# Kernel optimization log

Measured on AMD Instinct MI355X. Metric: run time of the kernel, lower is better.

The kernel has to match this reference:

```python
import jax, jax.numpy as jnp
import numpy as np

K = 3
PAD = 1
KK = K * K
GROUPS = 32  # min(32, dim) with dim=64
EPS = 1e-5


def _conv(x, w, pad):
    return jax.lax.conv_general_dilated(
        x, w, (1, 1), [(pad, pad), (pad, pad)],
        dimension_numbers=('NCHW', 'OIHW', 'NCHW'))


def _bilinear_gather(x, py, px):
    # x: (B,C,H,W); py,px: (B,KK,H,W) float sampling coords (zero pad outside)
    B, C, H, W = x.shape
    xf = x.reshape(B, C, H * W)
    y0f = jnp.floor(py)
    x0f = jnp.floor(px)
    wy1 = py - y0f  # fractional weights (differentiable path to offsets)
    wx1 = px - x0f
    y0 = y0f.astype(jnp.int32)
    x0 = x0f.astype(jnp.int32)

    def g(yi, xi):
        valid = (yi >= 0) & (yi < H) & (xi >= 0) & (xi < W)
        idx = (jnp.clip(yi, 0, H - 1) * W + jnp.clip(xi, 0, W - 1)).reshape(B, 1, -1)
        v = jnp.take_along_axis(xf, idx, axis=2).reshape(B, C, KK, H, W)
        return v * valid[:, None].astype(x.dtype)

    v00 = g(y0, x0)
    v01 = g(y0, x0 + 1)
    v10 = g(y0 + 1, x0)
    v11 = g(y0 + 1, x0 + 1)
    wy1e = wy1[:, None]
    wx1e = wx1[:, None]
    return (v00 * (1 - wy1e) * (1 - wx1e) + v01 * (1 - wy1e) * wx1e
            + v10 * wy1e * (1 - wx1e) + v11 * wy1e * wx1e)


def _forward(x, w_off1, w_off2, w_mask1, w_mask2, weight, bias, gamma, beta):
    B, C, H, W = x.shape
    # offset branch: 1x1 conv then KxK conv -> (B, 2*KK, H, W)
    off = _conv(_conv(x, w_off1, 0), w_off2, PAD).reshape(B, KK, 2, H, W)
    # mask branch -> sigmoid modulation (B, KK, H, W)
    mask = jax.nn.sigmoid(_conv(_conv(x, w_mask1, 0), w_mask2, PAD))
    # base kernel grid (torchvision deform_conv2d: pairs are (dy, dx) per tap)
    ky = jnp.repeat(jnp.arange(K) - PAD, K).astype(x.dtype)
    kx = jnp.tile(jnp.arange(K) - PAD, K).astype(x.dtype)
    py = off[:, :, 0] + jnp.arange(H, dtype=x.dtype)[None, None, :, None] + ky[None, :, None, None]
    px = off[:, :, 1] + jnp.arange(W, dtype=x.dtype)[None, None, None, :] + kx[None, :, None, None]
    samp = _bilinear_gather(x, py, px)  # (B, C, KK, H, W)
    # depthwise deformable conv: per-channel weight over KK taps, modulated by mask
    out = jnp.einsum('bkhw,ck,bckhw->bchw', mask, weight.reshape(C, KK), samp)
    out = out + bias[None, :, None, None]
    # GroupNorm(32, C)
    g = out.reshape(B, GROUPS, C // GROUPS, H, W)
    mu = g.mean(axis=(2, 3, 4), keepdims=True)
    var = g.var(axis=(2, 3, 4), keepdims=True)
    gn = ((g - mu) * jax.lax.rsqrt(var + EPS)).reshape(B, C, H, W)
    gn = gn * gamma[None, :, None, None] + beta[None, :, None, None]
    return jax.nn.gelu(gn, approximate=False)


def setup_inputs() -> dict:
    key = jax.random.key(0)
    ks = jax.random.split(key, 6)
    B, C, H, W = 4, 64, 128, 128
    x = jax.random.normal(ks[0], (B, C, H, W), dtype=jnp.float32)
    w_off1 = jax.random.normal(ks[1], (C, C, 1, 1), dtype=jnp.float32) * 0.05
    w_off2 = jax.random.normal(ks[2], (2 * KK, C, K, K), dtype=jnp.float32) * 0.02
    w_mask1 = jax.random.normal(ks[3], (C, C, 1, 1), dtype=jnp.float32) * 0.05
    w_mask2 = jax.random.normal(ks[4], (KK, C, K, K), dtype=jnp.float32) * 0.05
    bound = 1.0 / np.sqrt(KK)  # kaiming_uniform(a=1) for (C,1,K,K) -> fan_in=KK
    weight = jax.random.uniform(ks[5], (C, 1, K, K), dtype=jnp.float32,
                                minval=-bound, maxval=bound)
    bias = jnp.zeros((C,), dtype=jnp.float32)
    gamma = jnp.ones((C,), dtype=jnp.float32)
    beta = jnp.zeros((C,), dtype=jnp.float32)
    return {'x': x, 'w_off1': w_off1, 'w_off2': w_off2, 'w_mask1': w_mask1,
            'w_mask2': w_mask2, 'weight': weight, 'bias': bias,
            'gamma': gamma, 'beta': beta}


def reference(x, w_off1, w_off2, w_mask1, w_mask2, weight, bias, gamma, beta):
    return _forward(x, w_off1, w_off2, w_mask1, w_mask2, weight, bias, gamma, beta)
```

## Files before the change

### kernel.cpp

```cpp
#include <hip/hip_runtime.h>
#include <math.h>

#define B_  4
#define C_  64
#define H_  128
#define W_  128
#define HW_ (H_*W_)
#define NPIX_ (B_*HW_)
#define GROUPS_ 32

typedef __attribute__((ext_vector_type(8))) short short8;
typedef __attribute__((ext_vector_type(4))) float f32x4;

__device__ inline short f2bf_rne(float f) {
    unsigned u = __float_as_uint(f);
    unsigned r = (u + 0x7FFFu + ((u >> 16) & 1u)) >> 16;
    return (short)r;
}
__device__ inline short8 ld8(const short* p) {
    union { uint4 u; short8 s; } c;
    c.u = *(const uint4*)p;
    return c.s;
}

__global__ __launch_bounds__(256) void k01(const float* __restrict__ x,
                                           const float* __restrict__ w_off1,
                                           const float* __restrict__ w_mask1,
                                           const float* __restrict__ w_off2,
                                           const float* __restrict__ w_mask2,
                                           short* __restrict__ xtb,
                                           short* __restrict__ wc_hi) {
    if (blockIdx.x >= 1024) {
        int i = (blockIdx.x - 1024) * 256 + threadIdx.x;
        if (i < 32 * 576) {
            int cout = i / 576;
            int r    = i % 576;
            int pos  = r >> 6, ci = r & 63;
            float s = 0.f;
            if (cout < 18) {
                for (int cm = 0; cm < 64; cm++)
                    s += w_off2[(cout * 64 + cm) * 9 + pos] * w_off1[cm * 64 + ci];
            } else if (cout < 27) {
                for (int cm = 0; cm < 64; cm++)
                    s += w_mask2[((cout - 18) * 64 + cm) * 9 + pos] * w_mask1[cm * 64 + ci];
            }
            wc_hi[i] = f2bf_rne(s);
        }
        return;
    }
    int l   = threadIdx.x & 63;
    int wv  = threadIdx.x >> 6;
    int row = l >> 4, col = l & 15;
    int p0  = blockIdx.x * 64 + wv * 16;
    int b   = p0 >> 14;
    int hw  = p0 & (HW_ - 1);
    const float* xb = x + (size_t)b * C_ * HW_ + hw;
#pragma unroll
    for (int kb = 0; kb < 2; kb++) {
        int ci0 = kb * 32 + row * 8;
        float xv[8];
#pragma unroll
        for (int j = 0; j < 8; j++) xv[j] = xb[(ci0 + j) * HW_ + col];
        short8 a;
#pragma unroll
        for (int j = 0; j < 8; j++) a[j] = f2bf_rne(xv[j]);
        union { short8 s; uint4 u; } cv; cv.s = a;
        *(uint4*)(xtb + ((size_t)(p0 + col)) * 64 + ci0) = cv.u;
    }
}

__global__ __launch_bounds__(256, 2) void k2_mfma(const short* __restrict__ xtb,
                                                  const short* __restrict__ wc_hi,
                                                  float* __restrict__ offmask) {
    int l   = threadIdx.x & 63;
    int wv  = threadIdx.x >> 6;
    int row = l >> 4, col = l & 15;
    int blk = blockIdx.x;
    int h   = blk & 127;
    int pb  = blk * 128 + wv * 32;
    int w0  = (pb & 127);

    short8 wfr[18][2];
#pragma unroll
    for (int kb = 0; kb < 18; kb++) {
        int pos = kb >> 1;
        int ci0 = (kb & 1) * 32 + row * 8;
        int ko  = pos * 64 + ci0;
        wfr[kb][0] = ld8(wc_hi + (size_t)col * 576 + ko);
        wfr[kb][1] = ld8(wc_hi + (size_t)(col + 16) * 576 + ko);
    }

    const short8 zero = {0,0,0,0,0,0,0,0};
    f32x4 a00 = {0.f,0.f,0.f,0.f};
    f32x4 a01 = {0.f,0.f,0.f,0.f};
    f32x4 a10 = {0.f,0.f,0.f,0.f};
    f32x4 a11 = {0.f,0.f,0.f,0.f};

    short8 ca0, ca1;
    {
        const int dy = -1, dx = -1;
        int ci0 = row * 8;
#pragma unroll
        for (int mt = 0; mt < 2; mt++) {
            int pbase = pb + mt * 16 + col;
            int w = w0 + mt * 16 + col;
            bool valid = ((unsigned)(h + dy) < 128u) && ((unsigned)(w + dx) < 128u);
            int addr = valid ? (pbase + dy * 128 + dx) : pbase;
            short8 v = ld8(xtb + (size_t)addr * 64 + ci0);
            if (mt == 0) ca0 = valid ? v : zero; else ca1 = valid ? v : zero;
        }
    }

#pragma unroll
    for (int kb = 0; kb < 18; kb++) {
        short8 na0, na1;
        if (kb < 17) {
            const int kn = kb + 1;
            const int pos = kn >> 1;
            const int dy = pos / 3 - 1, dx = pos % 3 - 1;
            int ci0 = (kn & 1) * 32 + row * 8;
#pragma unroll
            for (int mt = 0; mt < 2; mt++) {
                int pbase = pb + mt * 16 + col;
                int w = w0 + mt * 16 + col;
                bool valid = ((unsigned)(h + dy) < 128u) && ((unsigned)(w + dx) < 128u);
                int addr = valid ? (pbase + dy * 128 + dx) : pbase;
                short8 v = ld8(xtb + (size_t)addr * 64 + ci0);
                if (mt == 0) na0 = valid ? v : zero; else na1 = valid ? v : zero;
            }
        }
        a00 = __builtin_amdgcn_mfma_f32_16x16x32_bf16(ca0, wfr[kb][0], a00, 0, 0, 0);
        a01 = __builtin_amdgcn_mfma_f32_16x16x32_bf16(ca0, wfr[kb][1], a01, 0, 0, 0);
        a10 = __builtin_amdgcn_mfma_f32_16x16x32_bf16(ca1, wfr[kb][0], a10, 0, 0, 0);
        a11 = __builtin_amdgcn_mfma_f32_16x16x32_bf16(ca1, wfr[kb][1], a11, 0, 0, 0);
        ca0 = na0; ca1 = na1;
    }

#pragma unroll
    for (int mt = 0; mt < 2; mt++) {
        f32x4 n0 = mt ? a10 : a00;
        f32x4 n1 = mt ? a11 : a01;
#pragma unroll
        for (int r = 0; r < 4; r++) {
            int p = pb + mt * 16 + row * 4 + r;
            float* om = offmask + (size_t)p * 32;
            om[col] = n0[r];
            if (col < 2)       om[16 + col] = n1[r];
            else if (col < 11) om[16 + col] = 1.f / (1.f + expf(-n1[r]));
        }
    }
}

__global__ __launch_bounds__(256) void k3_deform(const short* __restrict__ xtb,
                                                 const float* __restrict__ offmask,
                                                 const float* __restrict__ weight,
                                                 const float* __restrict__ bias,
                                                 unsigned short* __restrict__ out_pre,
                                                 float* __restrict__ partials) {
    __shared__ float wl[C_ * 9];
    __shared__ float bl[C_];
    __shared__ float lds_s[4][4][8];
    __shared__ float lds_ss[4][4][8];
    for (int i = threadIdx.x; i < C_ * 9; i += 256) wl[i] = weight[i];
    if (threadIdx.x < C_) bl[threadIdx.x] = bias[threadIdx.x];
    __syncthreads();

    int blk   = blockIdx.x;
    int xcd   = blk & 7;
    int slot  = blk >> 3;
    int b     = slot >> 5;
    int r     = (slot & 31) >> 1;
    int hrow  = slot & 1;
    int h     = xcd * 16 + r;
    int pl    = threadIdx.x >> 2;
    int chunk = threadIdx.x & 3;
    int c0    = chunk * 16;
    int w     = hrow * 64 + pl;
    int hw    = h * W_ + w;
    int P     = b * HW_ + hw;
    int slot_img = xcd * 32 + (slot & 31);

    float acc[16];
#pragma unroll
    for (int i = 0; i < 16; i++) acc[i] = 0.f;

    const float* po = offmask + (size_t)P * 32;
    const short* xb = xtb + (size_t)b * HW_ * 64;

    for (int k = 0; k < 9; k++) {
        float offy = po[2 * k];
        float offx = po[2 * k + 1];
        float mk   = po[18 + k];
        float py = offy + (float)h + (float)(k / 3 - 1);
        float px = offx + (float)w + (float)(k % 3 - 1);
        float y0f = floorf(py), x0f = floorf(px);
        int y0 = (int)y0f, x0 = (int)x0f;
        int y1 = y0 + 1,   x1 = x0 + 1;
        float wy1 = py - y0f, wx1 = px - x0f;
        float wy0 = 1.f - wy1, wx0 = 1.f - wx1;
        bool vy0 = ((unsigned)y0 < (unsigned)H_);
        bool vy1 = ((unsigned)y1 < (unsigned)H_);
        bool vx0 = ((unsigned)x0 < (unsigned)W_);
        bool vx1 = ((unsigned)x1 < (unsigned)W_);
        int cy0 = min(max(y0, 0), H_ - 1);
        int cy1 = min(max(y1, 0), H_ - 1);
        int cx0 = min(max(x0, 0), W_ - 1);
        int cx1 = min(max(x1, 0), W_ - 1);
        float b00 = wy0 * wx0 * ((vy0 && vx0) ? mk : 0.f);
        float b01 = wy0 * wx1 * ((vy0 && vx1) ? mk : 0.f);
        float b10 = wy1 * wx0 * ((vy1 && vx0) ? mk : 0.f);
        float b11 = wy1 * wx1 * ((vy1 && vx1) ? mk : 0.f);

        const short* p00 = xb + ((size_t)cy0 * W_ + cx0) * 64 + c0;
        const short* p01 = xb + ((size_t)cy0 * W_ + cx1) * 64 + c0;
        const short* p10 = xb + ((size_t)cy1 * W_ + cx0) * 64 + c0;
        const short* p11 = xb + ((size_t)cy1 * W_ + cx1) * 64 + c0;

#pragma unroll
        for (int half = 0; half < 2; half++) {
            uint4 u00 = *(const uint4*)(p00 + 8 * half);
            uint4 u01 = *(const uint4*)(p01 + 8 * half);
            uint4 u10 = *(const uint4*)(p10 + 8 * half);
            uint4 u11 = *(const uint4*)(p11 + 8 * half);
            unsigned a00[4] = {u00.x, u00.y, u00.z, u00.w};
            unsigned a01[4] = {u01.x, u01.y, u01.z, u01.w};
            unsigned a10[4] = {u10.x, u10.y, u10.z, u10.w};
            unsigned a11[4] = {u11.x, u11.y, u11.z, u11.w};
#pragma unroll
            for (int d = 0; d < 4; d++) {
                float s_lo = b00 * __uint_as_float(a00[d] << 16)
                           + b01 * __uint_as_float(a01[d] << 16)
                           + b10 * __uint_as_float(a10[d] << 16)
                           + b11 * __uint_as_float(a11[d] << 16);
                float s_hi = b00 * __uint_as_float(a00[d] & 0xFFFF0000u)
                           + b01 * __uint_as_float(a01[d] & 0xFFFF0000u)
                           + b10 * __uint_as_float(a10[d] & 0xFFFF0000u)
                           + b11 * __uint_as_float(a11[d] & 0xFFFF0000u);
                int c = 8 * half + 2 * d;
                acc[c]     += wl[(c0 + c) * 9 + k] * s_lo;
                acc[c + 1] += wl[(c0 + c + 1) * 9 + k] * s_hi;
            }
        }
    }

    unsigned short* op = out_pre + ((size_t)b * C_ + c0) * HW_ + hw;
#pragma unroll
    for (int c = 0; c < 16; c++) {
        acc[c] += bl[c0 + c];
        op[c * HW_] = (unsigned short)f2bf_rne(acc[c]);
    }

    float s8[8], ss8[8];
#pragma unroll
    for (int j = 0; j < 8; j++) {
        float a0 = acc[2 * j], a1 = acc[2 * j + 1];
        s8[j]  = a0 + a1;
        ss8[j] = a0 * a0 + a1 * a1;
    }
#pragma unroll
    for (int m = 4; m < 64; m <<= 1) {
#pragma unroll
        for (int j = 0; j < 8; j++) {
            s8[j]  += __shfl_xor(s8[j], m);
            ss8[j] += __shfl_xor(ss8[j], m);
        }
    }
    int lane = threadIdx.x & 63, wid = threadIdx.x >> 6;
    if (lane < 4) {
#pragma unroll
        for (int j = 0; j < 8; j++) {
            lds_s[wid][lane][j]  = s8[j];
            lds_ss[wid][lane][j] = ss8[j];
        }
    }
    __syncthreads();
    if (threadIdx.x < 32) {
        int g = threadIdx.x;
        int ch = g >> 3, j = g & 7;
        float S  = lds_s[0][ch][j] + lds_s[1][ch][j] + lds_s[2][ch][j] + lds_s[3][ch][j];
        float SS = lds_ss[0][ch][j] + lds_ss[1][ch][j] + lds_ss[2][ch][j] + lds_ss[3][ch][j];
        float2 v = make_float2(S, SS);
        *(float2*)(partials + (((size_t)(b * GROUPS_ + g)) * 256 + slot_img) * 2) = v;
    }
}

__global__ __launch_bounds__(256) void k4_reduce(const float* __restrict__ partials,
                                                 float* __restrict__ stats) {
    int bg = blockIdx.x;
    float2 v = ((const float2*)partials)[bg * 256 + threadIdx.x];
    float s = v.x, ss = v.y;
#pragma unroll
    for (int m = 1; m < 64; m <<= 1) {
        s  += __shfl_xor(s, m);
        ss += __shfl_xor(ss, m);
    }
    __shared__ float ls[8];
    int lane = threadIdx.x & 63, wid = threadIdx.x >> 6;
    if (lane == 0) { ls[wid] = s; ls[4 + wid] = ss; }
    __syncthreads();
    if (threadIdx.x == 0) {
        float S  = ls[0] + ls[1] + ls[2] + ls[3];
        float SS = ls[4] + ls[5] + ls[6] + ls[7];
        const float inv = 1.f / (2.f * HW_);
        float mean = S * inv;
        float var  = SS * inv - mean * mean;
        stats[bg * 2]     = mean;
        stats[bg * 2 + 1] = rsqrtf(var + 1e-5f);
    }
}

__global__ __launch_bounds__(256) void k5_norm_gelu(const unsigned short* __restrict__ out_pre,
                                                    const float* __restrict__ stats,
                                                    const float* __restrict__ gamma,
                                                    const float* __restrict__ beta,
                                                    float* __restrict__ out) {
    int i = blockIdx.x * 256 + threadIdx.x;
    int e = i << 3;
    int c = (e >> 14) & (C_ - 1);
    int b = e >> 20;
    int bg = b * GROUPS_ + (c >> 1);
    float mean = stats[bg * 2];
    float rstd = stats[bg * 2 + 1];
    float ga = gamma[c] * rstd;
    float be = beta[c] - mean * ga;
    uint4 v = ((const uint4*)out_pre)[i];
    unsigned dw[4] = {v.x, v.y, v.z, v.w};
    float o[8];
#pragma unroll
    for (int d = 0; d < 4; d++) {
        float lo = __uint_as_float(dw[d] << 16);
        float hi = __uint_as_float(dw[d] & 0xFFFF0000u);
        float t0 = lo * ga + be;
        float t1 = hi * ga + be;
        o[2 * d]     = 0.5f * t0 * (1.f + erff(t0 * 0.70710678118654752f));
        o[2 * d + 1] = 0.5f * t1 * (1.f + erff(t1 * 0.70710678118654752f));
    }
    ((float4*)out)[2 * i]     = make_float4(o[0], o[1], o[2], o[3]);
    ((float4*)out)[2 * i + 1] = make_float4(o[4], o[5], o[6], o[7]);
}

extern "C" void kernel_launch(void* const* d_in, const int* in_sizes, int n_in,
                              void* d_out, int out_size, void* d_ws, size_t ws_size,
                              hipStream_t stream) {
    const float* x       = (const float*)d_in[0];
    const float* w_off1  = (const float*)d_in[1];
    const float* w_off2  = (const float*)d_in[2];
    const float* w_mask1 = (const float*)d_in[3];
    const float* w_mask2 = (const float*)d_in[4];
    const float* weight  = (const float*)d_in[5];
    const float* bias    = (const float*)d_in[6];
    const float* gamma   = (const float*)d_in[7];
    const float* beta    = (const float*)d_in[8];
    float* out = (float*)d_out;

    char* ws = (char*)d_ws;
    size_t o = 0;
    short* wc_hi = (short*)(ws + o); o += 32 * 576 * 2;
    o = (o + 255) & ~(size_t)255;
    short* xtb               = (short*)(ws + o);          o += (size_t)NPIX_ * 64 * 2;
    float* offmask           = (float*)(ws + o);          o += (size_t)NPIX_ * 32 * 4;
    unsigned short* out_pre  = (unsigned short*)(ws + o); o += (size_t)NPIX_ * 64 * 2;
    float* partials          = (float*)(ws + o);          o += (size_t)128 * 256 * 2 * 4;
    float* stats             = (float*)(ws + o);          o += 256 * 4;

    hipLaunchKernelGGL(k01, dim3(1024 + 72), dim3(256), 0, stream,
                       x, w_off1, w_mask1, w_off2, w_mask2, xtb, wc_hi);
    hipLaunchKernelGGL(k2_mfma, dim3(NPIX_ / 128), dim3(256), 0, stream,
                       xtb, wc_hi, offmask);
    hipLaunchKernelGGL(k3_deform, dim3(NPIX_ / 64), dim3(256), 0, stream,
                       xtb, offmask, weight, bias, out_pre, partials);
    hipLaunchKernelGGL(k4_reduce, dim3(B_ * GROUPS_), dim3(256), 0, stream,
                       partials, stats);
    hipLaunchKernelGGL(k5_norm_gelu, dim3(NPIX_ * 64 / 8 / 256), dim3(256), 0, stream,
                       out_pre, stats, gamma, beta, out);
}
```

Baseline: 135.6 us.

## Fuse offset/mask MFMA conv into deform kernel and use atomic GroupNorm stats

Computes the combined offset/mask convolution with MFMA inside the deformable kernel, staging the per-pixel offsets and masks in LDS instead of writing and rereading an offmask buffer through global memory. Replaces the partials buffer and separate reduce kernel with atomic accumulation of the GroupNorm sums. The accumulator is zeroed in the first kernel, and the final norm kernel derives mean and rstd itself. This removes two launches and a global round trip, at the cost of more per-block work in the fused kernel, weight fragments reloaded per step, and atomic contention on 256 floats.

Measured after the change: 145.2 us. 7.0% more time.

```diff
diff --git a/kernel.cpp b/kernel.cpp
--- a/kernel.cpp
+++ b/kernel.cpp
@@ -29,9 +29,11 @@
                                            const float* __restrict__ w_off2,
                                            const float* __restrict__ w_mask2,
                                            short* __restrict__ xtb,
-                                           short* __restrict__ wc_hi) {
+                                           short* __restrict__ wc_hi,
+                                           float* __restrict__ stats_acc) {
     if (blockIdx.x >= 1024) {
         int i = (blockIdx.x - 1024) * 256 + threadIdx.x;
+        if (blockIdx.x == 1024) stats_acc[threadIdx.x] = 0.f;
         if (i < 32 * 576) {
             int cout = i / 576;
             int r    = i % 576;
@@ -69,101 +71,19 @@
     }
 }
 
-__global__ __launch_bounds__(256, 2) void k2_mfma(const short* __restrict__ xtb,
-                                                  const short* __restrict__ wc_hi,
-                                                  float* __restrict__ offmask) {
-    int l   = threadIdx.x & 63;
-    int wv  = threadIdx.x >> 6;
-    int row = l >> 4, col = l & 15;
-    int blk = blockIdx.x;
-    int h   = blk & 127;
-    int pb  = blk * 128 + wv * 32;
-    int w0  = (pb & 127);
-
-    short8 wfr[18][2];
-#pragma unroll
-    for (int kb = 0; kb < 18; kb++) {
-        int pos = kb >> 1;
-        int ci0 = (kb & 1) * 32 + row * 8;
-        int ko  = pos * 64 + ci0;
-        wfr[kb][0] = ld8(wc_hi + (size_t)col * 576 + ko);
-        wfr[kb][1] = ld8(wc_hi + (size_t)(col + 16) * 576 + ko);
-    }
-
-    const short8 zero = {0,0,0,0,0,0,0,0};
-    f32x4 a00 = {0.f,0.f,0.f,0.f};
-    f32x4 a01 = {0.f,0.f,0.f,0.f};
-    f32x4 a10 = {0.f,0.f,0.f,0.f};
-    f32x4 a11 = {0.f,0.f,0.f,0.f};
-
-    short8 ca0, ca1;
-    {
-        const int dy = -1, dx = -1;
-        int ci0 = row * 8;
-#pragma unroll
-        for (int mt = 0; mt < 2; mt++) {
-            int pbase = pb + mt * 16 + col;
-            int w = w0 + mt * 16 + col;
-            bool valid = ((unsigned)(h + dy) < 128u) && ((unsigned)(w + dx) < 128u);
-            int addr = valid ? (pbase + dy * 128 + dx) : pbase;
-            short8 v = ld8(xtb + (size_t)addr * 64 + ci0);
-            if (mt == 0) ca0 = valid ? v : zero; else ca1 = valid ? v : zero;
-        }
-    }
-
-#pragma unroll
-    for (int kb = 0; kb < 18; kb++) {
-        short8 na0, na1;
-        if (kb < 17) {
-            const int kn = kb + 1;
-            const int pos = kn >> 1;
-            const int dy = pos / 3 - 1, dx = pos % 3 - 1;
-            int ci0 = (kn & 1) * 32 + row * 8;
-#pragma unroll
-            for (int mt = 0; mt < 2; mt++) {
-                int pbase = pb + mt * 16 + col;
-                int w = w0 + mt * 16 + col;
-                bool valid = ((unsigned)(h + dy) < 128u) && ((unsigned)(w + dx) < 128u);
-                int addr = valid ? (pbase + dy * 128 + dx) : pbase;
-                short8 v = ld8(xtb + (size_t)addr * 64 + ci0);
-                if (mt == 0) na0 = valid ? v : zero; else na1 = valid ? v : zero;
-            }
-        }
-        a00 = __builtin_amdgcn_mfma_f32_16x16x32_bf16(ca0, wfr[kb][0], a00, 0, 0, 0);
-        a01 = __builtin_amdgcn_mfma_f32_16x16x32_bf16(ca0, wfr[kb][1], a01, 0, 0, 0);
-        a10 = __builtin_amdgcn_mfma_f32_16x16x32_bf16(ca1, wfr[kb][0], a10, 0, 0, 0);
-        a11 = __builtin_amdgcn_mfma_f32_16x16x32_bf16(ca1, wfr[kb][1], a11, 0, 0, 0);
-        ca0 = na0; ca1 = na1;
-    }
-
-#pragma unroll
-    for (int mt = 0; mt < 2; mt++) {
-        f32x4 n0 = mt ? a10 : a00;
-        f32x4 n1 = mt ? a11 : a01;
-#pragma unroll
-        for (int r = 0; r < 4; r++) {
-            int p = pb + mt * 16 + row * 4 + r;
-            float* om = offmask + (size_t)p * 32;
-            om[col] = n0[r];
-            if (col < 2)       om[16 + col] = n1[r];
-            else if (col < 11) om[16 + col] = 1.f / (1.f + expf(-n1[r]));
-        }
-    }
-}
-
-__global__ __launch_bounds__(256) void k3_deform(const short* __restrict__ xtb,
-                                                 const float* __restrict__ offmask,
-                                                 const float* __restrict__ weight,
-                                                 const float* __restrict__ bias,
-                                                 unsigned short* __restrict__ out_pre,
-                                                 float* __restrict__ partials) {
+__global__ __launch_bounds__(256) void k3_fused(const short* __restrict__ xtb,
+                                                const short* __restrict__ wc_hi,
+                                                const float* __restrict__ weight,
+                                                const float* __restrict__ bias,
+                                                unsigned short* __restrict__ out_pre,
+                                                float* __restrict__ stats_acc) {
     __shared__ float wl[C_ * 9];
     __shared__ float bl[C_];
+    __shared__ float pom[64][28];
     __shared__ float lds_s[4][4][8];
     __shared__ float lds_ss[4][4][8];
     for (int i = threadIdx.x; i < C_ * 9; i += 256) wl[i] = weight[i];
     if (threadIdx.x < C_) bl[threadIdx.x] = bias[threadIdx.x];
-    __syncthreads();
 
     int blk   = blockIdx.x;
     int xcd   = blk & 7;
@@ -172,25 +92,74 @@
     int r     = (slot & 31) >> 1;
     int hrow  = slot & 1;
     int h     = xcd * 16 + r;
+
+    {
+        int l   = threadIdx.x & 63;
+        int wv  = threadIdx.x >> 6;
+        int row = l >> 4, col = l & 15;
+        int wA    = hrow * 64 + wv * 16 + col;
+        int pbase = b * HW_ + h * W_ + wA;
+
+        const short8 zero8 = {0,0,0,0,0,0,0,0};
+        f32x4 acc0 = {0.f,0.f,0.f,0.f};
+        f32x4 acc1 = {0.f,0.f,0.f,0.f};
+
+        short8 ca, cb0, cb1;
+        {
+            int ci0 = row * 8;
+            bool valid = ((unsigned)(h - 1) < 128u) && ((unsigned)(wA - 1) < 128u);
+            int addr = valid ? (pbase - 128 - 1) : pbase;
+            short8 v = ld8(xtb + (size_t)addr * 64 + ci0);
+            ca  = valid ? v : zero8;
+            cb0 = ld8(wc_hi + (size_t)col * 576 + ci0);
+            cb1 = ld8(wc_hi + (size_t)(col + 16) * 576 + ci0);
+        }
+#pragma unroll
+        for (int kb = 0; kb < 18; kb++) {
+            short8 na, nb0, nb1;
+            if (kb < 17) {
+                const int kn  = kb + 1;
+                const int pos = kn >> 1;
+                const int dy  = pos / 3 - 1, dx = pos % 3 - 1;
+                int ci0 = (kn & 1) * 32 + row * 8;
+                bool valid = ((unsigned)(h + dy) < 128u) && ((unsigned)(wA + dx) < 128u);
+                int addr = valid ? (pbase + dy * 128 + dx) : pbase;
+                short8 v = ld8(xtb + (size_t)addr * 64 + ci0);
+                na  = valid ? v : zero8;
+                nb0 = ld8(wc_hi + (size_t)col * 576 + pos * 64 + ci0);
+                nb1 = ld8(wc_hi + (size_t)(col + 16) * 576 + pos * 64 + ci0);
+            }
+            acc0 = __builtin_amdgcn_mfma_f32_16x16x32_bf16(ca, cb0, acc0, 0, 0, 0);
+            acc1 = __builtin_amdgcn_mfma_f32_16x16x32_bf16(ca, cb1, acc1, 0, 0, 0);
+            ca = na; cb0 = nb0; cb1 = nb1;
+        }
+
+#pragma unroll
+        for (int rr = 0; rr < 4; rr++) {
+            int pxl = wv * 16 + row * 4 + rr;
+            pom[pxl][col] = acc0[rr];
+            if (col < 2)       pom[pxl][16 + col] = acc1[rr];
+            else if (col < 11) pom[pxl][16 + col] = 1.f / (1.f + expf(-acc1[rr]));
+        }
+    }
+    __syncthreads();
+
     int pl    = threadIdx.x >> 2;
     int chunk = threadIdx.x & 3;
     int c0    = chunk * 16;
     int w     = hrow * 64 + pl;
     int hw    = h * W_ + w;
-    int P     = b * HW_ + hw;
-    int slot_img = xcd * 32 + (slot & 31);
 
     float acc[16];
 #pragma unroll
     for (int i = 0; i < 16; i++) acc[i] = 0.f;
 
-    const float* po = offmask + (size_t)P * 32;
     const short* xb = xtb + (size_t)b * HW_ * 64;
 
     for (int k = 0; k < 9; k++) {
-        float offy = po[2 * k];
-        float offx = po[2 * k + 1];
-        float mk   = po[18 + k];
+        float offy = pom[pl][2 * k];
+        float offx = pom[pl][2 * k + 1];
+        float mk   = pom[pl][18 + k];
         float py = offy + (float)h + (float)(k / 3 - 1);
         float px = offx + (float)w + (float)(k % 3 - 1);
         float y0f = floorf(py), x0f = floorf(px);
@@ -279,38 +248,13 @@
         int ch = g >> 3, j = g & 7;
         float S  = lds_s[0][ch][j] + lds_s[1][ch][j] + lds_s[2][ch][j] + lds_s[3][ch][j];
         float SS = lds_ss[0][ch][j] + lds_ss[1][ch][j] + lds_ss[2][ch][j] + lds_ss[3][ch][j];
-        float2 v = make_float2(S, SS);
-        *(float2*)(partials + (((size_t)(b * GROUPS_ + g)) * 256 + slot_img) * 2) = v;
-    }
-}
-
-__global__ __launch_bounds__(256) void k4_reduce(const float* __restrict__ partials,
-                                                 float* __restrict__ stats) {
-    int bg = blockIdx.x;
-    float2 v = ((const float2*)partials)[bg * 256 + threadIdx.x];
-    float s = v.x, ss = v.y;
-#pragma unroll
-    for (int m = 1; m < 64; m <<= 1) {
-        s  += __shfl_xor(s, m);
-        ss += __shfl_xor(ss, m);
-    }
-    __shared__ float ls[8];
-    int lane = threadIdx.x & 63, wid = threadIdx.x >> 6;
-    if (lane == 0) { ls[wid] = s; ls[4 + wid] = ss; }
-    __syncthreads();
-    if (threadIdx.x == 0) {
-        float S  = ls[0] + ls[1] + ls[2] + ls[3];
-        float SS = ls[4] + ls[5] + ls[6] + ls[7];
-        const float inv = 1.f / (2.f * HW_);
-        float mean = S * inv;
-        float var  = SS * inv - mean * mean;
-        stats[bg * 2]     = mean;
-        stats[bg * 2 + 1] = rsqrtf(var + 1e-5f);
+        atomicAdd(&stats_acc[(b * GROUPS_ + g) * 2],     S);
+        atomicAdd(&stats_acc[(b * GROUPS_ + g) * 2 + 1], SS);
     }
 }
 
 __global__ __launch_bounds__(256) void k5_norm_gelu(const unsigned short* __restrict__ out_pre,
-                                                    const float* __restrict__ stats,
+                                                    const float* __restrict__ stats_acc,
                                                     const float* __restrict__ gamma,
                                                     const float* __restrict__ beta,
                                                     float* __restrict__ out) {
@@ -319,8 +263,12 @@
     int c = (e >> 14) & (C_ - 1);
     int b = e >> 20;
     int bg = b * GROUPS_ + (c >> 1);
-    float mean = stats[bg * 2];
-    float rstd = stats[bg * 2 + 1];
+    float S  = stats_acc[bg * 2];
+    float SS = stats_acc[bg * 2 + 1];
+    const float inv = 1.f / (2.f * HW_);
+    float mean = S * inv;
+    float var  = SS * inv - mean * mean;
+    float rstd = rsqrtf(var + 1e-5f);
     float ga = gamma[c] * rstd;
     float be = beta[c] - mean * ga;
     uint4 v = ((const uint4*)out_pre)[i];
@@ -358,19 +306,13 @@
     short* wc_hi = (short*)(ws + o); o += 32 * 576 * 2;
     o = (o + 255) & ~(size_t)255;
     short* xtb               = (short*)(ws + o);          o += (size_t)NPIX_ * 64 * 2;
-    float* offmask           = (float*)(ws + o);          o += (size_t)NPIX_ * 32 * 4;
     unsigned short* out_pre  = (unsigned short*)(ws + o); o += (size_t)NPIX_ * 64 * 2;
-    float* partials          = (float*)(ws + o);          o += (size_t)128 * 256 * 2 * 4;
-    float* stats             = (float*)(ws + o);          o += 256 * 4;
+    float* stats_acc         = (float*)(ws + o);          o += 256 * 4;
 
     hipLaunchKernelGGL(k01, dim3(1024 + 72), dim3(256), 0, stream,
-                       x, w_off1, w_mask1, w_off2, w_mask2, xtb, wc_hi);
-    hipLaunchKernelGGL(k2_mfma, dim3(NPIX_ / 128), dim3(256), 0, stream,
-                       xtb, wc_hi, offmask);
-    hipLaunchKernelGGL(k3_deform, dim3(NPIX_ / 64), dim3(256), 0, stream,
-                       xtb, offmask, weight, bias, out_pre, partials);
-    hipLaunchKernelGGL(k4_reduce, dim3(B_ * GROUPS_), dim3(256), 0, stream,
-                       partials, stats);
+                       x, w_off1, w_mask1, w_off2, w_mask2, xtb, wc_hi, stats_acc);
+    hipLaunchKernelGGL(k3_fused, dim3(NPIX_ / 64), dim3(256), 0, stream,
+                       xtb, wc_hi, weight, bias, out_pre, stats_acc);
     hipLaunchKernelGGL(k5_norm_gelu, dim3(NPIX_ * 64 / 8 / 256), dim3(256), 0, stream,
-                       out_pre, stats, gamma, beta, out);
-}
+                       out_pre, stats_acc, gamma, beta, out);
+}
```

## Split deform channels over more threads and fuse GroupNorm stats via atomics

Applied to the files above, without the earlier changes.

The deformable conv kernel now gives each thread 8 channels instead of 16 and uses 32 pixels per block. This doubles the grid and halves per-thread registers, with launch bounds requesting higher occupancy. The separate reduction kernel is removed: per-block group sums are accumulated with atomicAdd into a buffer zeroed in the first kernel, and the normalize kernel derives mean and rstd itself. This saves one launch and the partials round-trip, at the cost of more offset/coordinate recomputation per thread, atomic contention, and nondeterministic summation order.

Result: slower. 231.7 us (+70.9%).

```diff
diff --git a/kernel.cpp b/kernel.cpp
--- a/kernel.cpp
+++ b/kernel.cpp
@@ -29,9 +29,11 @@
                                            const float* __restrict__ w_off2,
                                            const float* __restrict__ w_mask2,
                                            short* __restrict__ xtb,
-                                           short* __restrict__ wc_hi) {
+                                           short* __restrict__ wc_hi,
+                                           float* __restrict__ stats_acc) {
     if (blockIdx.x >= 1024) {
         int i = (blockIdx.x - 1024) * 256 + threadIdx.x;
+        if (blockIdx.x == 1024) stats_acc[threadIdx.x] = 0.f;
         if (i < 32 * 576) {
             int cout = i / 576;
             int r    = i % 576;
@@ -151,16 +153,16 @@
     }
 }
 
-__global__ __launch_bounds__(256) void k3_deform(const short* __restrict__ xtb,
-                                                 const float* __restrict__ offmask,
-                                                 const float* __restrict__ weight,
-                                                 const float* __restrict__ bias,
-                                                 unsigned short* __restrict__ out_pre,
-                                                 float* __restrict__ partials) {
+__global__ __launch_bounds__(256, 8) void k3_deform(const short* __restrict__ xtb,
+                                                    const float* __restrict__ offmask,
+                                                    const float* __restrict__ weight,
+                                                    const float* __restrict__ bias,
+                                                    unsigned short* __restrict__ out_pre,
+                                                    float* __restrict__ stats_acc) {
     __shared__ float wl[C_ * 9];
     __shared__ float bl[C_];
-    __shared__ float lds_s[4][4][8];
-    __shared__ float lds_ss[4][4][8];
+    __shared__ float lds_s[4][8][4];
+    __shared__ float lds_ss[4][8][4];
     for (int i = threadIdx.x; i < C_ * 9; i += 256) wl[i] = weight[i];
     if (threadIdx.x < C_) bl[threadIdx.x] = bias[threadIdx.x];
     __syncthreads();
@@ -168,21 +170,21 @@
     int blk   = blockIdx.x;
     int xcd   = blk & 7;
     int slot  = blk >> 3;
-    int b     = slot >> 5;
-    int r     = (slot & 31) >> 1;
-    int hrow  = slot & 1;
+    int b     = slot >> 6;
+    int s2    = slot & 63;
+    int r     = s2 >> 2;
+    int q     = s2 & 3;
     int h     = xcd * 16 + r;
-    int pl    = threadIdx.x >> 2;
-    int chunk = threadIdx.x & 3;
-    int c0    = chunk * 16;
-    int w     = hrow * 64 + pl;
+    int pl    = threadIdx.x >> 3;
+    int chunk = threadIdx.x & 7;
+    int c0    = chunk * 8;
+    int w     = q * 32 + pl;
     int hw    = h * W_ + w;
     int P     = b * HW_ + hw;
-    int slot_img = xcd * 32 + (slot & 31);
-
-    float acc[16];
-#pragma unroll
-    for (int i = 0; i < 16; i++) acc[i] = 0.f;
+
+    float acc[8];
+#pragma unroll
+    for (int i = 0; i < 8; i++) acc[i] = 0.f;
 
     const float* po = offmask + (size_t)P * 32;
     const short* xb = xtb + (size_t)b * HW_ * 64;
@@ -211,106 +213,73 @@
         float b10 = wy1 * wx0 * ((vy1 && vx0) ? mk : 0.f);
         float b11 = wy1 * wx1 * ((vy1 && vx1) ? mk : 0.f);
 
-        const short* p00 = xb + ((size_t)cy0 * W_ + cx0) * 64 + c0;
-        const short* p01 = xb + ((size_t)cy0 * W_ + cx1) * 64 + c0;
-        const short* p10 = xb + ((size_t)cy1 * W_ + cx0) * 64 + c0;
-        const short* p11 = xb + ((size_t)cy1 * W_ + cx1) * 64 + c0;
-
-#pragma unroll
-        for (int half = 0; half < 2; half++) {
-            uint4 u00 = *(const uint4*)(p00 + 8 * half);
-            uint4 u01 = *(const uint4*)(p01 + 8 * half);
-            uint4 u10 = *(const uint4*)(p10 + 8 * half);
-            uint4 u11 = *(const uint4*)(p11 + 8 * half);
-            unsigned a00[4] = {u00.x, u00.y, u00.z, u00.w};
-            unsigned a01[4] = {u01.x, u01.y, u01.z, u01.w};
-            unsigned a10[4] = {u10.x, u10.y, u10.z, u10.w};
-            unsigned a11[4] = {u11.x, u11.y, u11.z, u11.w};
-#pragma unroll
-            for (int d = 0; d < 4; d++) {
-                float s_lo = b00 * __uint_as_float(a00[d] << 16)
-                           + b01 * __uint_as_float(a01[d] << 16)
-                           + b10 * __uint_as_float(a10[d] << 16)
-                           + b11 * __uint_as_float(a11[d] << 16);
-                float s_hi = b00 * __uint_as_float(a00[d] & 0xFFFF0000u)
-                           + b01 * __uint_as_float(a01[d] & 0xFFFF0000u)
-                           + b10 * __uint_as_float(a10[d] & 0xFFFF0000u)
-                           + b11 * __uint_as_float(a11[d] & 0xFFFF0000u);
-                int c = 8 * half + 2 * d;
-                acc[c]     += wl[(c0 + c) * 9 + k] * s_lo;
-                acc[c + 1] += wl[(c0 + c + 1) * 9 + k] * s_hi;
-            }
+        uint4 u00 = *(const uint4*)(xb + ((size_t)cy0 * W_ + cx0) * 64 + c0);
+        uint4 u01 = *(const uint4*)(xb + ((size_t)cy0 * W_ + cx1) * 64 + c0);
+        uint4 u10 = *(const uint4*)(xb + ((size_t)cy1 * W_ + cx0) * 64 + c0);
+        uint4 u11 = *(const uint4*)(xb + ((size_t)cy1 * W_ + cx1) * 64 + c0);
+        unsigned a00[4] = {u00.x, u00.y, u00.z, u00.w};
+        unsigned a01[4] = {u01.x, u01.y, u01.z, u01.w};
+        unsigned a10[4] = {u10.x, u10.y, u10.z, u10.w};
+        unsigned a11[4] = {u11.x, u11.y, u11.z, u11.w};
+#pragma unroll
+        for (int d = 0; d < 4; d++) {
+            float s_lo = b00 * __uint_as_float(a00[d] << 16)
+                       + b01 * __uint_as_float(a01[d] << 16)
+                       + b10 * __uint_as_float(a10[d] << 16)
+                       + b11 * __uint_as_float(a11[d] << 16);
+            float s_hi = b00 * __uint_as_float(a00[d] & 0xFFFF0000u)
+                       + b01 * __uint_as_float(a01[d] & 0xFFFF0000u)
+                       + b10 * __uint_as_float(a10[d] & 0xFFFF0000u)
+                       + b11 * __uint_as_float(a11[d] & 0xFFFF0000u);
+            int c = 2 * d;
+            acc[c]     += wl[(c0 + c) * 9 + k] * s_lo;
+            acc[c + 1] += wl[(c0 + c + 1) * 9 + k] * s_hi;
         }
     }
 
     unsigned short* op = out_pre + ((size_t)b * C_ + c0) * HW_ + hw;
 #pragma unroll
-    for (int c = 0; c < 16; c++) {
+    for (int c = 0; c < 8; c++) {
         acc[c] += bl[c0 + c];
         op[c * HW_] = (unsigned short)f2bf_rne(acc[c]);
     }
 
-    float s8[8], ss8[8];
-#pragma unroll
-    for (int j = 0; j < 8; j++) {
+    float s4[4], ss4[4];
+#pragma unroll
+    for (int j = 0; j < 4; j++) {
         float a0 = acc[2 * j], a1 = acc[2 * j + 1];
-        s8[j]  = a0 + a1;
-        ss8[j] = a0 * a0 + a1 * a1;
-    }
-#pragma unroll
-    for (int m = 4; m < 64; m <<= 1) {
-#pragma unroll
-        for (int j = 0; j < 8; j++) {
-            s8[j]  += __shfl_xor(s8[j], m);
-            ss8[j] += __shfl_xor(ss8[j], m);
+        s4[j]  = a0 + a1;
+        ss4[j] = a0 * a0 + a1 * a1;
+    }
+#pragma unroll
+    for (int m = 8; m < 64; m <<= 1) {
+#pragma unroll
+        for (int j = 0; j < 4; j++) {
+            s4[j]  += __shfl_xor(s4[j], m);
+            ss4[j] += __shfl_xor(ss4[j], m);
         }
     }
     int lane = threadIdx.x & 63, wid = threadIdx.x >> 6;
-    if (lane < 4) {
-#pragma unroll
-        for (int j = 0; j < 8; j++) {
-            lds_s[wid][lane][j]  = s8[j];
-            lds_ss[wid][lane][j] = ss8[j];
+    if (lane < 8) {
+#pragma unroll
+        for (int j = 0; j < 4; j++) {
+            lds_s[wid][lane][j]  = s4[j];
+            lds_ss[wid][lane][j] = ss4[j];
         }
     }
     __syncthreads();
     if (threadIdx.x < 32) {
-        int g = threadIdx.x;
-        int ch = g >> 3, j = g & 7;
+        int g  = threadIdx.x;
+        int ch = g >> 2, j = g & 3;
         float S  = lds_s[0][ch][j] + lds_s[1][ch][j] + lds_s[2][ch][j] + lds_s[3][ch][j];
         float SS = lds_ss[0][ch][j] + lds_ss[1][ch][j] + lds_ss[2][ch][j] + lds_ss[3][ch][j];
-        float2 v = make_float2(S, SS);
-        *(float2*)(partials + (((size_t)(b * GROUPS_ + g)) * 256 + slot_img) * 2) = v;
-    }
-}
-
-__global__ __launch_bounds__(256) void k4_reduce(const float* __restrict__ partials,
-                                                 float* __restrict__ stats) {
-    int bg = blockIdx.x;
-    float2 v = ((const float2*)partials)[bg * 256 + threadIdx.x];
-    float s = v.x, ss = v.y;
-#pragma unroll
-    for (int m = 1; m < 64; m <<= 1) {
-        s  += __shfl_xor(s, m);
-        ss += __shfl_xor(ss, m);
-    }
-    __shared__ float ls[8];
-    int lane = threadIdx.x & 63, wid = threadIdx.x >> 6;
-    if (lane == 0) { ls[wid] = s; ls[4 + wid] = ss; }
-    __syncthreads();
-    if (threadIdx.x == 0) {
-        float S  = ls[0] + ls[1] + ls[2] + ls[3];
-        float SS = ls[4] + ls[5] + ls[6] + ls[7];
-        const float inv = 1.f / (2.f * HW_);
-        float mean = S * inv;
-        float var  = SS * inv - mean * mean;
-        stats[bg * 2]     = mean;
-        stats[bg * 2 + 1] = rsqrtf(var + 1e-5f);
+        atomicAdd(&stats_acc[(b * GROUPS_ + g) * 2],     S);
+        atomicAdd(&stats_acc[(b * GROUPS_ + g) * 2 + 1], SS);
     }
 }
 
 __global__ __launch_bounds__(256) void k5_norm_gelu(const unsigned short* __restrict__ out_pre,
-                                                    const float* __restrict__ stats,
+                                                    const float* __restrict__ stats_acc,
                                                     const float* __restrict__ gamma,
                                                     const float* __restrict__ beta,
                                                     float* __restrict__ out) {
@@ -319,8 +288,12 @@
     int c = (e >> 14) & (C_ - 1);
     int b = e >> 20;
     int bg = b * GROUPS_ + (c >> 1);
-    float mean = stats[bg * 2];
-    float rstd = stats[bg * 2 + 1];
+    float S  = stats_acc[bg * 2];
+    float SS = stats_acc[bg * 2 + 1];
+    const float inv = 1.f / (2.f * HW_);
+    float mean = S * inv;
+    float var  = SS * inv - mean * mean;
+    float rstd = rsqrtf(var + 1e-5f);
     float ga = gamma[c] * rstd;
     float be = beta[c] - mean * ga;
     uint4 v = ((const uint4*)out_pre)[i];
@@ -360,17 +333,14 @@
     short* xtb               = (short*)(ws + o);          o += (size_t)NPIX_ * 64 * 2;
     float* offmask           = (float*)(ws + o);          o += (size_t)NPIX_ * 32 * 4;
     unsigned short* out_pre  = (unsigned short*)(ws + o); o += (size_t)NPIX_ * 64 * 2;
-    float* partials          = (float*)(ws + o);          o += (size_t)128 * 256 * 2 * 4;
-    float* stats             = (float*)(ws + o);          o += 256 * 4;
+    float* stats_acc         = (float*)(ws + o);          o += 256 * 4;
 
     hipLaunchKernelGGL(k01, dim3(1024 + 72), dim3(256), 0, stream,
-                       x, w_off1, w_mask1, w_off2, w_mask2, xtb, wc_hi);
+                       x, w_off1, w_mask1, w_off2, w_mask2, xtb, wc_hi, stats_acc);
     hipLaunchKernelGGL(k2_mfma, dim3(NPIX_ / 128), dim3(256), 0, stream,
                        xtb, wc_hi, offmask);
-    hipLaunchKernelGGL(k3_deform, dim3(NPIX_ / 64), dim3(256), 0, stream,
-                       xtb, offmask, weight, bias, out_pre, partials);
-    hipLaunchKernelGGL(k4_reduce, dim3(B_ * GROUPS_), dim3(256), 0, stream,
-                       partials, stats);
+    hipLaunchKernelGGL(k3_deform, dim3(NPIX_ / 32), dim3(256), 0, stream,
+                       xtb, offmask, weight, bias, out_pre, stats_acc);
     hipLaunchKernelGGL(k5_norm_gelu, dim3(NPIX_ * 64 / 8 / 256), dim3(256), 0, stream,
-                       out_pre, stats, gamma, beta, out);
-}
+                       out_pre, stats_acc, gamma, beta, out);
+}
```

## Stage offset/mask rows in LDS and software-pipeline bilinear gathers across taps

Applied to the files above, without the earlier changes.

The deformable-conv kernel now loads the block's 64 pixels of offset/mask data into padded shared memory with coalesced float4 loads, replacing per-thread strided global reads. The 9-tap loop is fully unrolled and double-buffered, so the eight gather loads for tap k+1 are issued before tap k's interpolation math. This is meant to hide gather latency and cut uncoalesced offset reads. The cost is higher register pressure from holding two sets of gathered data, which could reduce occupancy.

Result: slower. 148.4 us (+9.4%).

```diff
diff --git a/kernel.cpp b/kernel.cpp
--- a/kernel.cpp
+++ b/kernel.cpp
@@ -151,6 +151,37 @@
     }
 }
 
+__device__ __forceinline__ void prep_k(const float* __restrict__ pr, int h, int w, int k,
+                                       float& b00, float& b01, float& b10, float& b11,
+                                       int& o00, int& o01, int& o10, int& o11) {
+    float offy = pr[2 * k];
+    float offx = pr[2 * k + 1];
+    float mk   = pr[18 + k];
+    float py = offy + (float)(h + k / 3 - 1);
+    float px = offx + (float)(w + k % 3 - 1);
+    float y0f = floorf(py), x0f = floorf(px);
+    int y0 = (int)y0f, x0 = (int)x0f;
+    int y1 = y0 + 1,   x1 = x0 + 1;
+    float wy1 = py - y0f, wx1 = px - x0f;
+    float wy0 = 1.f - wy1, wx0 = 1.f - wx1;
+    bool vy0 = ((unsigned)y0 < (unsigned)H_);
+    bool vy1 = ((unsigned)y1 < (unsigned)H_);
+    bool vx0 = ((unsigned)x0 < (unsigned)W_);
+    bool vx1 = ((unsigned)x1 < (unsigned)W_);
+    int cy0 = min(max(y0, 0), H_ - 1);
+    int cy1 = min(max(y1, 0), H_ - 1);
+    int cx0 = min(max(x0, 0), W_ - 1);
+    int cx1 = min(max(x1, 0), W_ - 1);
+    b00 = wy0 * wx0 * ((vy0 && vx0) ? mk : 0.f);
+    b01 = wy0 * wx1 * ((vy0 && vx1) ? mk : 0.f);
+    b10 = wy1 * wx0 * ((vy1 && vx0) ? mk : 0.f);
+    b11 = wy1 * wx1 * ((vy1 && vx1) ? mk : 0.f);
+    o00 = (cy0 * W_ + cx0) * 64;
+    o01 = (cy0 * W_ + cx1) * 64;
+    o10 = (cy1 * W_ + cx0) * 64;
+    o11 = (cy1 * W_ + cx1) * 64;
+}
+
 __global__ __launch_bounds__(256) void k3_deform(const short* __restrict__ xtb,
                                                  const float* __restrict__ offmask,
                                                  const float* __restrict__ weight,
@@ -159,11 +190,11 @@
                                                  float* __restrict__ partials) {
     __shared__ float wl[C_ * 9];
     __shared__ float bl[C_];
+    __shared__ float pom[64][33];
     __shared__ float lds_s[4][4][8];
     __shared__ float lds_ss[4][4][8];
     for (int i = threadIdx.x; i < C_ * 9; i += 256) wl[i] = weight[i];
     if (threadIdx.x < C_) bl[threadIdx.x] = bias[threadIdx.x];
-    __syncthreads();
 
     int blk   = blockIdx.x;
     int xcd   = blk & 7;
@@ -172,74 +203,82 @@
     int r     = (slot & 31) >> 1;
     int hrow  = slot & 1;
     int h     = xcd * 16 + r;
+    int P0    = b * HW_ + h * W_ + hrow * 64;
+
+    {
+        const float4* src = (const float4*)(offmask + (size_t)P0 * 32);
+        float4 v0 = src[threadIdx.x];
+        float4 v1 = src[threadIdx.x + 256];
+        int px0 = threadIdx.x >> 3;
+        int cb  = (threadIdx.x & 7) * 4;
+        pom[px0][cb + 0] = v0.x; pom[px0][cb + 1] = v0.y;
+        pom[px0][cb + 2] = v0.z; pom[px0][cb + 3] = v0.w;
+        pom[px0 + 32][cb + 0] = v1.x; pom[px0 + 32][cb + 1] = v1.y;
+        pom[px0 + 32][cb + 2] = v1.z; pom[px0 + 32][cb + 3] = v1.w;
+    }
+    __syncthreads();
+
     int pl    = threadIdx.x >> 2;
     int chunk = threadIdx.x & 3;
     int c0    = chunk * 16;
     int w     = hrow * 64 + pl;
     int hw    = h * W_ + w;
-    int P     = b * HW_ + hw;
     int slot_img = xcd * 32 + (slot & 31);
 
+    const short* xb = xtb + (size_t)b * HW_ * 64 + c0;
+    const float* pr = &pom[pl][0];
+
     float acc[16];
 #pragma unroll
     for (int i = 0; i < 16; i++) acc[i] = 0.f;
 
-    const float* po = offmask + (size_t)P * 32;
-    const short* xb = xtb + (size_t)b * HW_ * 64;
-
+    float B00, B01, B10, B11;
+    uint4 d00a, d00b, d01a, d01b, d10a, d10b, d11a, d11b;
+    {
+        int o00, o01, o10, o11;
+        prep_k(pr, h, w, 0, B00, B01, B10, B11, o00, o01, o10, o11);
+        d00a = *(const uint4*)(xb + o00); d00b = *(const uint4*)(xb + o00 + 8);
+        d01a = *(const uint4*)(xb + o01); d01b = *(const uint4*)(xb + o01 + 8);
+        d10a = *(const uint4*)(xb + o10); d10b = *(const uint4*)(xb + o10 + 8);
+        d11a = *(const uint4*)(xb + o11); d11b = *(const uint4*)(xb + o11 + 8);
+    }
+
+#pragma unroll
     for (int k = 0; k < 9; k++) {
-        float offy = po[2 * k];
-        float offx = po[2 * k + 1];
-        float mk   = po[18 + k];
-        float py = offy + (float)h + (float)(k / 3 - 1);
-        float px = offx + (float)w + (float)(k % 3 - 1);
-        float y0f = floorf(py), x0f = floorf(px);
-        int y0 = (int)y0f, x0 = (int)x0f;
-        int y1 = y0 + 1,   x1 = x0 + 1;
-        float wy1 = py - y0f, wx1 = px - x0f;
-        float wy0 = 1.f - wy1, wx0 = 1.f - wx1;
-        bool vy0 = ((unsigned)y0 < (unsigned)H_);
-        bool vy1 = ((unsigned)y1 < (unsigned)H_);
-        bool vx0 = ((unsigned)x0 < (unsigned)W_);
-        bool vx1 = ((unsigned)x1 < (unsigned)W_);
-        int cy0 = min(max(y0, 0), H_ - 1);
-        int cy1 = min(max(y1, 0), H_ - 1);
-        int cx0 = min(max(x0, 0), W_ - 1);
-        int cx1 = min(max(x1, 0), W_ - 1);
-        float b00 = wy0 * wx0 * ((vy0 && vx0) ? mk : 0.f);
-        float b01 = wy0 * wx1 * ((vy0 && vx1) ? mk : 0.f);
-        float b10 = wy1 * wx0 * ((vy1 && vx0) ? mk : 0.f);
-        float b11 = wy1 * wx1 * ((vy1 && vx1) ? mk : 0.f);
-
-        const short* p00 = xb + ((size_t)cy0 * W_ + cx0) * 64 + c0;
-        const short* p01 = xb + ((size_t)cy0 * W_ + cx1) * 64 + c0;
-        const short* p10 = xb + ((size_t)cy1 * W_ + cx0) * 64 + c0;
-        const short* p11 = xb + ((size_t)cy1 * W_ + cx1) * 64 + c0;
-
-#pragma unroll
-        for (int half = 0; half < 2; half++) {
-            uint4 u00 = *(const uint4*)(p00 + 8 * half);
-            uint4 u01 = *(const uint4*)(p01 + 8 * half);
-            uint4 u10 = *(const uint4*)(p10 + 8 * half);
-            uint4 u11 = *(const uint4*)(p11 + 8 * half);
-            unsigned a00[4] = {u00.x, u00.y, u00.z, u00.w};
-            unsigned a01[4] = {u01.x, u01.y, u01.z, u01.w};
-            unsigned a10[4] = {u10.x, u10.y, u10.z, u10.w};
-            unsigned a11[4] = {u11.x, u11.y, u11.z, u11.w};
-#pragma unroll
-            for (int d = 0; d < 4; d++) {
-                float s_lo = b00 * __uint_as_float(a00[d] << 16)
-                           + b01 * __uint_as_float(a01[d] << 16)
-                           + b10 * __uint_as_float(a10[d] << 16)
-                           + b11 * __uint_as_float(a11[d] << 16);
-                float s_hi = b00 * __uint_as_float(a00[d] & 0xFFFF0000u)
-                           + b01 * __uint_as_float(a01[d] & 0xFFFF0000u)
-                           + b10 * __uint_as_float(a10[d] & 0xFFFF0000u)
-                           + b11 * __uint_as_float(a11[d] & 0xFFFF0000u);
-                int c = 8 * half + 2 * d;
+        float N00 = 0.f, N01 = 0.f, N10 = 0.f, N11 = 0.f;
+        uint4 n00a, n00b, n01a, n01b, n10a, n10b, n11a, n11b;
+        if (k < 8) {
+            int o00, o01, o10, o11;
+            prep_k(pr, h, w, k + 1, N00, N01, N10, N11, o00, o01, o10, o11);
+            n00a = *(const uint4*)(xb + o00); n00b = *(const uint4*)(xb + o00 + 8);
+            n01a = *(const uint4*)(xb + o01); n01b = *(const uint4*)(xb + o01 + 8);
+            n10a = *(const uint4*)(xb + o10); n10b = *(const uint4*)(xb + o10 + 8);
+            n11a = *(const uint4*)(xb + o11); n11b = *(const uint4*)(xb + o11 + 8);
+        }
+        {
+            unsigned q00[8] = {d00a.x, d00a.y, d00a.z, d00a.w, d00b.x, d00b.y, d00b.z, d00b.w};
+            unsigned q01[8] = {d01a.x, d01a.y, d01a.z, d01a.w, d01b.x, d01b.y, d01b.z, d01b.w};
+            unsigned q10[8] = {d10a.x, d10a.y, d10a.z, d10a.w, d10b.x, d10b.y, d10b.z, d10b.w};
+            unsigned q11[8] = {d11a.x, d11a.y, d11a.z, d11a.w, d11b.x, d11b.y, d11b.z, d11b.w};
+#pragma unroll
+            for (int d = 0; d < 8; d++) {
+                float s_lo = B00 * __uint_as_float(q00[d] << 16)
+                           + B01 * __uint_as_float(q01[d] << 16)
+                           + B10 * __uint_as_float(q10[d] << 16)
+                           + B11 * __uint_as_float(q11[d] << 16);
+                float s_hi = B00 * __uint_as_float(q00[d] & 0xFFFF0000u)
+                           + B01 * __uint_as_float(q01[d] & 0xFFFF0000u)
+                           + B10 * __uint_as_float(q10[d] & 0xFFFF0000u)
+                           + B11 * __uint_as_float(q11[d] & 0xFFFF0000u);
+                int c = 2 * d;
                 acc[c]     += wl[(c0 + c) * 9 + k] * s_lo;
                 acc[c + 1] += wl[(c0 + c + 1) * 9 + k] * s_hi;
             }
+        }
+        if (k < 8) {
+            d00a = n00a; d00b = n00b; d01a = n01a; d01b = n01b;
+            d10a = n10a; d10b = n10b; d11a = n11a; d11b = n11b;
+            B00 = N00; B01 = N01; B10 = N10; B11 = N11;
         }
     }
 
```
